# Kernel tuning notes

Measured on AMD Instinct MI355X. Metric: run time of the kernel, lower is better.

The kernel has to match this reference:

```python
import jax, jax.numpy as jnp
import numpy as np

N, F, E, C = 50000, 128, 800000, 10

def setup_inputs() -> dict:
    key = jax.random.key(0)
    ks = jax.random.split(key, 16)
    s = 1.0 / np.sqrt(F)
    def u(k, shape):
        return jax.random.uniform(k, shape, jnp.float32, -s, s)
    inp = {
        "x": jax.random.normal(ks[0], (N, F), jnp.float32),
        "edge_index": jax.random.randint(ks[1], (2, E), 0, N),
    }
    for i, p in enumerate(["1", "2"]):
        b = 2 + i * 5
        inp["W" + p] = u(ks[b], (F, F))          # EvolveGCNO initial_weight
        inp["wih" + p] = u(ks[b + 1], (3 * F, F))  # GRU input weights (r,z,n)
        inp["whh" + p] = u(ks[b + 2], (3 * F, F))  # GRU hidden weights
        inp["bih" + p] = u(ks[b + 3], (3 * F,))
        inp["bhh" + p] = u(ks[b + 4], (3 * F,))
    inp["lin_w"] = u(ks[12], (C, F))
    inp["lin_b"] = u(ks[13], (C,))
    return inp

def gru_step(x, h, wih, whh, bih, bhh):
    # torch.nn.GRU single step; gate order r, z, n
    gi = x @ wih.T + bih
    gh = h @ whh.T + bhh
    ir, iz, inn = jnp.split(gi, 3, axis=-1)
    hr, hz, hn = jnp.split(gh, 3, axis=-1)
    r = jax.nn.sigmoid(ir + hr)
    z = jax.nn.sigmoid(iz + hz)
    n = jnp.tanh(inn + r * hn)
    return (1.0 - z) * n + z * h

def gcn_conv(W, x, src, dst):
    # GCNConv_Fixed_W: gcn_norm with self-loops, then aggregate (x @ W)
    n = x.shape[0]
    loop = jnp.arange(n)
    s = jnp.concatenate([src, loop])
    d = jnp.concatenate([dst, loop])
    deg = jax.ops.segment_sum(jnp.ones(s.shape[0], x.dtype), d, num_segments=n)
    dinv = jnp.where(deg > 0, jax.lax.rsqrt(deg), 0.0)
    norm = dinv[s] * dinv[d]                 # [E+N]
    xw = x @ W                               # [N, F]
    return jax.ops.segment_sum(norm[:, None] * xw[s], d, num_segments=n)

def evolve_gcno(x, src, dst, W0, wih, whh, bih, bhh):
    # weight evolved by GRU with input = hidden = current weight
    W = gru_step(W0, W0, wih, whh, bih, bhh)
    return gcn_conv(W, x, src, dst)

def reference(x, edge_index, W1, wih1, whh1, bih1, bhh1,
              W2, wih2, whh2, bih2, bhh2, lin_w, lin_b):
    src, dst = edge_index[0], edge_index[1]
    h = jax.nn.relu(evolve_gcno(x, src, dst, W1, wih1, whh1, bih1, bhh1))
    # dropout is identity in eval mode
    h = jax.nn.relu(evolve_gcno(h, src, dst, W2, wih2, whh2, bih2, bhh2))
    logits = h @ lin_w.T + lin_b
    return jax.nn.log_softmax(logits, axis=1)
```

## Files before the change

kernel.cpp:

```cpp
#include <hip/hip_runtime.h>
#include <cstddef>
#include <cstdint>

#define F 128
#define C_OUT 10
#define SB 256

typedef short bf16x8 __attribute__((ext_vector_type(8)));
typedef float f32x4  __attribute__((ext_vector_type(4)));

__device__ __forceinline__ unsigned pack_bf16x2(float a, float b) {
  unsigned ua = __float_as_uint(a);
  unsigned ub = __float_as_uint(b);
  ua = (ua + 0x7FFFu + ((ua >> 16) & 1u)) >> 16;
  ub = (ub + 0x7FFFu + ((ub >> 16) & 1u)) >> 16;
  return ua | (ub << 16);
}
__device__ __forceinline__ float unpk_lo(unsigned p) { return __uint_as_float(p << 16); }
__device__ __forceinline__ float unpk_hi(unsigned p) { return __uint_as_float(p & 0xFFFF0000u); }
__device__ __forceinline__ unsigned short bf16_rne(float f) {
  unsigned u = __float_as_uint(f);
  return (unsigned short)((u + 0x7FFFu + ((u >> 16) & 1u)) >> 16);
}

__global__ void gru_evolve2_k(const float* __restrict__ W01, const float* __restrict__ wih1,
                              const float* __restrict__ whh1, const float* __restrict__ bih1,
                              const float* __restrict__ bhh1,
                              const float* __restrict__ W02, const float* __restrict__ wih2,
                              const float* __restrict__ whh2, const float* __restrict__ bih2,
                              const float* __restrict__ bhh2,
                              unsigned short* __restrict__ Bhi1, unsigned short* __restrict__ Blo1,
                              unsigned short* __restrict__ Bhi2, unsigned short* __restrict__ Blo2,
                              int* __restrict__ counts, int n) {
  if ((int)blockIdx.x >= 128) {
    int i = ((int)blockIdx.x - 128) * SB + threadIdx.x;
    if (i < n) counts[i] = 0;
    return;
  }
  int t = blockIdx.x * 256 + threadIdx.x;
  int layer = t >> 14;
  int tt = t & 16383;
  const float* W0  = layer ? W02  : W01;
  const float* wih = layer ? wih2 : wih1;
  const float* whh = layer ? whh2 : whh1;
  const float* bih = layer ? bih2 : bih1;
  const float* bhh = layer ? bhh2 : bhh1;
  unsigned short* Bhi = layer ? Bhi2 : Bhi1;
  unsigned short* Blo = layer ? Blo2 : Blo1;
  int i = tt >> 7, j = tt & 127;
  const float4* w0r = (const float4*)(W0 + (size_t)i * F);
  float gi[3], gh[3];
#pragma unroll
  for (int g = 0; g < 3; ++g) {
    const float4* wr = (const float4*)(wih + (size_t)(g * F + j) * F);
    const float4* hr = (const float4*)(whh + (size_t)(g * F + j) * F);
    float si = 0.f, sh = 0.f;
    for (int k = 0; k < F / 4; ++k) {
      float4 a = w0r[k];
      float4 b = wr[k];
      float4 c = hr[k];
      si += a.x * b.x + a.y * b.y + a.z * b.z + a.w * b.w;
      sh += a.x * c.x + a.y * c.y + a.z * c.z + a.w * c.w;
    }
    gi[g] = si + bih[g * F + j];
    gh[g] = sh + bhh[g * F + j];
  }
  float r = 1.0f / (1.0f + expf(-(gi[0] + gh[0])));
  float z = 1.0f / (1.0f + expf(-(gi[1] + gh[1])));
  float nn = tanhf(gi[2] + r * gh[2]);
  float val = (1.0f - z) * nn + z * W0[(size_t)i * F + j];

  unsigned u = __float_as_uint(val);
  unsigned short hi = (unsigned short)(u >> 16);
  float lo_f = val - __uint_as_float(u & 0xFFFF0000u);
  unsigned short lo = bf16_rne(lo_f);
  int kstep = i >> 5, kl = i & 31;
  int lane = (kl >> 3) * 16 + (j & 15);
  int tile = j >> 4;
  int idx = ((kstep * 8 + tile) * 64 + lane) * 8 + (kl & 7);
  Bhi[idx] = hi;
  Blo[idx] = lo;
}

__global__ void count_rank_k(const int* __restrict__ dst, int* __restrict__ counts,
                             int* __restrict__ rank, int E) {
  int e = blockIdx.x * blockDim.x + threadIdx.x;
  if (e < E) rank[e] = atomicAdd(&counts[dst[e]], 1);
}

__global__ void scan_local_k(const int* __restrict__ counts, int* __restrict__ incl,
                             int* __restrict__ blocksum, int n) {
  __shared__ int sh[SB];
  int gid = blockIdx.x * SB + threadIdx.x;
  int v = (gid < n) ? counts[gid] : 0;
  sh[threadIdx.x] = v;
  __syncthreads();
  for (int off = 1; off < SB; off <<= 1) {
    int t = 0;
    if ((int)threadIdx.x >= off) t = sh[threadIdx.x - off];
    __syncthreads();
    if ((int)threadIdx.x >= off) sh[threadIdx.x] += t;
    __syncthreads();
  }
  if (gid < n) incl[gid] = sh[threadIdx.x];
  if (threadIdx.x == SB - 1) blocksum[blockIdx.x] = sh[SB - 1];
}

__global__ void scan_blocks_k(int* __restrict__ blocksum, int nb) {
  __shared__ int sh[SB];
  int v = ((int)threadIdx.x < nb) ? blocksum[threadIdx.x] : 0;
  sh[threadIdx.x] = v;
  __syncthreads();
  for (int off = 1; off < SB; off <<= 1) {
    int t = 0;
    if ((int)threadIdx.x >= off) t = sh[threadIdx.x - off];
    __syncthreads();
    if ((int)threadIdx.x >= off) sh[threadIdx.x] += t;
    __syncthreads();
  }
  if ((int)threadIdx.x < nb) blocksum[threadIdx.x] = sh[threadIdx.x] - v;
}

__global__ void scan_finish_k(const int* __restrict__ counts, const int* __restrict__ incl,
                              const int* __restrict__ blocksum, int* __restrict__ rowptr,
                              float* __restrict__ dinv, int n) {
  int gid = blockIdx.x * SB + threadIdx.x;
  if (gid >= n) return;
  int c = counts[gid];
  int inc = blocksum[blockIdx.x] + incl[gid];
  rowptr[gid] = inc - c;
  dinv[gid] = rsqrtf((float)c + 1.0f);
  if (gid == n - 1) rowptr[n] = inc;
}

__global__ void fill_k(const int* __restrict__ src, const int* __restrict__ dst,
                       const int* __restrict__ rank, const int* __restrict__ rowptr,
                       int* __restrict__ csr_src, int E) {
  int e = blockIdx.x * blockDim.x + threadIdx.x;
  if (e < E) {
    int d = dst[e];
    csr_src[rowptr[d] + rank[e]] = src[e];
  }
}

__global__ void gemm_mfma_k(const float* __restrict__ X,
                            const unsigned short* __restrict__ Bhi,
                            const unsigned short* __restrict__ Blo,
                            const float* __restrict__ dinv, unsigned* __restrict__ Y,
                            int nrows) {
  int wid = (int)((blockIdx.x * blockDim.x + threadIdx.x) >> 6);
  int lane = threadIdx.x & 63;
  int ng = (nrows + 15) >> 4;
  if (wid >= ng) return;
  int g = __builtin_amdgcn_readfirstlane(wid);
  int q = lane >> 4, m = lane & 15;
  int rowA = g * 16 + m;
  if (rowA >= nrows) rowA = nrows - 1;

  f32x4 acc[8];
#pragma unroll
  for (int t = 0; t < 8; ++t) { acc[t].x = 0.f; acc[t].y = 0.f; acc[t].z = 0.f; acc[t].w = 0.f; }

#pragma unroll
  for (int s = 0; s < 4; ++s) {
    const float* xp = X + (size_t)rowA * F + s * 32 + q * 8;
    float4 xa = *(const float4*)xp;
    float4 xb = *(const float4*)(xp + 4);
    float xv[8] = {xa.x, xa.y, xa.z, xa.w, xb.x, xb.y, xb.z, xb.w};
    bf16x8 xhi, xlo;
#pragma unroll
    for (int j = 0; j < 8; ++j) {
      unsigned u = __float_as_uint(xv[j]);
      xhi[j] = (short)(u >> 16);
      float lf = xv[j] - __uint_as_float(u & 0xFFFF0000u);
      xlo[j] = (short)bf16_rne(lf);
    }
#pragma unroll
    for (int t = 0; t < 8; ++t) {
      size_t boff = ((size_t)(s * 8 + t) * 64 + lane) * 8;
      bf16x8 wh = *(const bf16x8*)(Bhi + boff);
      bf16x8 wl = *(const bf16x8*)(Blo + boff);
      acc[t] = __builtin_amdgcn_mfma_f32_16x16x32_bf16(wh, xhi, acc[t], 0, 0, 0);
      acc[t] = __builtin_amdgcn_mfma_f32_16x16x32_bf16(wh, xlo, acc[t], 0, 0, 0);
      acc[t] = __builtin_amdgcn_mfma_f32_16x16x32_bf16(wl, xhi, acc[t], 0, 0, 0);
    }
  }

  int row = g * 16 + m;
  if (row < nrows) {
    float dd = dinv[row];
    unsigned* yr = Y + (size_t)row * 64 + q * 2;
#pragma unroll
    for (int t = 0; t < 8; ++t) {
      uint2 o;
      o.x = pack_bf16x2(dd * acc[t].x, dd * acc[t].y);
      o.y = pack_bf16x2(dd * acc[t].z, dd * acc[t].w);
      *(uint2*)(yr + t * 8) = o;
    }
  }
}

template <bool FUSE_LOGITS>
__global__ void agg_bf16_k(const int* __restrict__ rowptr, const int* __restrict__ csr_src,
                           const float* __restrict__ dinv, const unsigned* __restrict__ xwp,
                           float* __restrict__ hout,
                           const float* __restrict__ lw, const float* __restrict__ lb,
                           float* __restrict__ outp, int n) {
  int wave = (int)((blockIdx.x * blockDim.x + threadIdx.x) >> 6);
  int lane = threadIdx.x & 63;
  if (wave >= n) return;
  int node = __builtin_amdgcn_readfirstlane(wave);
  float dd = dinv[node];
  unsigned um = xwp[(size_t)node * 64 + lane];
  float accx = unpk_lo(um), accy = unpk_hi(um);
  int b = rowptr[node], e = rowptr[node + 1];
  int i = b;
  for (; i + 8 <= e; i += 8) {
    int s0 = csr_src[i + 0], s1 = csr_src[i + 1], s2 = csr_src[i + 2], s3 = csr_src[i + 3];
    int s4 = csr_src[i + 4], s5 = csr_src[i + 5], s6 = csr_src[i + 6], s7 = csr_src[i + 7];
    unsigned u0 = xwp[(size_t)s0 * 64 + lane];
    unsigned u1 = xwp[(size_t)s1 * 64 + lane];
    unsigned u2 = xwp[(size_t)s2 * 64 + lane];
    unsigned u3 = xwp[(size_t)s3 * 64 + lane];
    unsigned u4 = xwp[(size_t)s4 * 64 + lane];
    unsigned u5 = xwp[(size_t)s5 * 64 + lane];
    unsigned u6 = xwp[(size_t)s6 * 64 + lane];
    unsigned u7 = xwp[(size_t)s7 * 64 + lane];
    accx += unpk_lo(u0); accy += unpk_hi(u0);
    accx += unpk_lo(u1); accy += unpk_hi(u1);
    accx += unpk_lo(u2); accy += unpk_hi(u2);
    accx += unpk_lo(u3); accy += unpk_hi(u3);
    accx += unpk_lo(u4); accy += unpk_hi(u4);
    accx += unpk_lo(u5); accy += unpk_hi(u5);
    accx += unpk_lo(u6); accy += unpk_hi(u6);
    accx += unpk_lo(u7); accy += unpk_hi(u7);
  }
  for (; i < e; ++i) {
    int s = csr_src[i];
    unsigned u = xwp[(size_t)s * 64 + lane];
    accx += unpk_lo(u); accy += unpk_hi(u);
  }
  float hx = fmaxf(dd * accx, 0.f);
  float hy = fmaxf(dd * accy, 0.f);
  if (!FUSE_LOGITS) {
    float2 r; r.x = hx; r.y = hy;
    ((float2*)hout)[(size_t)node * 64 + lane] = r;
  } else {
    float acc[C_OUT];
    const float2* lw2 = (const float2*)lw;
#pragma unroll
    for (int c = 0; c < C_OUT; ++c) {
      float2 w = lw2[(size_t)c * 64 + lane];
      float v = hx * w.x + hy * w.y;
#pragma unroll
      for (int off = 1; off < 64; off <<= 1) v += __shfl_xor(v, off);
      acc[c] = v + lb[c];
    }
    float mx = acc[0];
#pragma unroll
    for (int c = 1; c < C_OUT; ++c) mx = fmaxf(mx, acc[c]);
    float s = 0.f;
#pragma unroll
    for (int c = 0; c < C_OUT; ++c) s += expf(acc[c] - mx);
    float lse = mx + logf(s);
#pragma unroll
    for (int c = 0; c < C_OUT; ++c)
      if (lane == c) outp[(size_t)node * C_OUT + c] = acc[c] - lse;
  }
}

extern "C" void kernel_launch(void* const* d_in, const int* in_sizes, int n_in,
                              void* d_out, int out_size, void* d_ws, size_t ws_size,
                              hipStream_t stream) {
  const float* x    = (const float*)d_in[0];
  const int*   ei   = (const int*)d_in[1];
  const float* W1   = (const float*)d_in[2];
  const float* wih1 = (const float*)d_in[3];
  const float* whh1 = (const float*)d_in[4];
  const float* bih1 = (const float*)d_in[5];
  const float* bhh1 = (const float*)d_in[6];
  const float* W2   = (const float*)d_in[7];
  const float* wih2 = (const float*)d_in[8];
  const float* whh2 = (const float*)d_in[9];
  const float* bih2 = (const float*)d_in[10];
  const float* bhh2 = (const float*)d_in[11];
  const float* lw   = (const float*)d_in[12];
  const float* lb   = (const float*)d_in[13];
  float* out = (float*)d_out;

  int N = in_sizes[0] / F;
  int E = in_sizes[1] / 2;
  const int* src = ei;
  const int* dst = ei + E;
  int nb = (N + SB - 1) / SB;
  int ng = (N + 15) / 16;

  float* ws   = (float*)d_ws;
  unsigned* bufA = (unsigned*)ws;
  float* bufB = ws + (size_t)N * F / 2;
  float* dinv = bufB + (size_t)N * F;
  unsigned short* Bhi1 = (unsigned short*)(dinv + N);
  unsigned short* Blo1 = Bhi1 + F * F;
  unsigned short* Bhi2 = Blo1 + F * F;
  unsigned short* Blo2 = Bhi2 + F * F;
  int* counts = (int*)(Blo2 + F * F);
  int* rowptr = counts + N;
  int* rank   = rowptr + N + 1;
  int* incl   = rank + E;
  int* blocksum = incl + N;
  int* csr_src = blocksum + 256;

  gru_evolve2_k<<<128 + nb, 256, 0, stream>>>(W1, wih1, whh1, bih1, bhh1,
                                              W2, wih2, whh2, bih2, bhh2,
                                              Bhi1, Blo1, Bhi2, Blo2, counts, N);

  count_rank_k<<<(E + 255) / 256, 256, 0, stream>>>(dst, counts, rank, E);
  scan_local_k<<<nb, SB, 0, stream>>>(counts, incl, blocksum, N);
  scan_blocks_k<<<1, SB, 0, stream>>>(blocksum, nb);
  scan_finish_k<<<nb, SB, 0, stream>>>(counts, incl, blocksum, rowptr, dinv, N);
  fill_k<<<(E + 255) / 256, 256, 0, stream>>>(src, dst, rank, rowptr, csr_src, E);

  gemm_mfma_k<<<(ng + 3) / 4, 256, 0, stream>>>(x, Bhi1, Blo1, dinv, bufA, N);
  agg_bf16_k<false><<<(N + 3) / 4, 256, 0, stream>>>(rowptr, csr_src, dinv, bufA, bufB,
                                                     nullptr, nullptr, nullptr, N);

  gemm_mfma_k<<<(ng + 3) / 4, 256, 0, stream>>>(bufB, Bhi2, Blo2, dinv, bufA, N);
  agg_bf16_k<true><<<(N + 3) / 4, 256, 0, stream>>>(rowptr, csr_src, dinv, bufA, nullptr,
                                                    lw, lb, out, N);
}
```

Before: 289.2 us.

## Split wave into four edge groups with 16-byte gathers; fuse block-scan into finish

Measured after the change: 294.1 us. No clear change (+1.7%).

```diff
diff --git a/kernel.cpp b/kernel.cpp
--- a/kernel.cpp
+++ b/kernel.cpp
@@ -106,10 +106,14 @@
   if (threadIdx.x == SB - 1) blocksum[blockIdx.x] = sh[SB - 1];
 }
 
-__global__ void scan_blocks_k(int* __restrict__ blocksum, int nb) {
+__global__ void scan_finish_k(const int* __restrict__ counts, const int* __restrict__ incl,
+                              const int* __restrict__ blocksum, int* __restrict__ rowptr,
+                              float* __restrict__ dinv, int n, int nb) {
   __shared__ int sh[SB];
+  __shared__ int orig[SB];
   int v = ((int)threadIdx.x < nb) ? blocksum[threadIdx.x] : 0;
   sh[threadIdx.x] = v;
+  orig[threadIdx.x] = v;
   __syncthreads();
   for (int off = 1; off < SB; off <<= 1) {
     int t = 0;
@@ -118,16 +122,11 @@
     if ((int)threadIdx.x >= off) sh[threadIdx.x] += t;
     __syncthreads();
   }
-  if ((int)threadIdx.x < nb) blocksum[threadIdx.x] = sh[threadIdx.x] - v;
-}
-
-__global__ void scan_finish_k(const int* __restrict__ counts, const int* __restrict__ incl,
-                              const int* __restrict__ blocksum, int* __restrict__ rowptr,
-                              float* __restrict__ dinv, int n) {
+  int myoff = sh[blockIdx.x] - orig[blockIdx.x];
   int gid = blockIdx.x * SB + threadIdx.x;
   if (gid >= n) return;
   int c = counts[gid];
-  int inc = blocksum[blockIdx.x] + incl[gid];
+  int inc = myoff + incl[gid];
   rowptr[gid] = inc - c;
   dinv[gid] = rsqrtf((float)c + 1.0f);
   if (gid == n - 1) rowptr[n] = inc;
@@ -210,50 +209,74 @@
   int lane = threadIdx.x & 63;
   if (wave >= n) return;
   int node = __builtin_amdgcn_readfirstlane(wave);
+  int q = lane >> 4, m = lane & 15;
   float dd = dinv[node];
-  unsigned um = xwp[(size_t)node * 64 + lane];
-  float accx = unpk_lo(um), accy = unpk_hi(um);
+  float a0 = 0.f, a1 = 0.f, a2 = 0.f, a3 = 0.f, a4 = 0.f, a5 = 0.f, a6 = 0.f, a7 = 0.f;
+
+#define ADD8(U)                                        \
+  do {                                                 \
+    a0 += unpk_lo((U).x); a1 += unpk_hi((U).x);        \
+    a2 += unpk_lo((U).y); a3 += unpk_hi((U).y);        \
+    a4 += unpk_lo((U).z); a5 += unpk_hi((U).z);        \
+    a6 += unpk_lo((U).w); a7 += unpk_hi((U).w);        \
+  } while (0)
+
+  {
+    uint4 u = *(const uint4*)(xwp + (size_t)node * 64 + m * 4);
+    if (q != 0) { u.x = 0u; u.y = 0u; u.z = 0u; u.w = 0u; }
+    ADD8(u);
+  }
+
   int b = rowptr[node], e = rowptr[node + 1];
   int i = b;
   for (; i + 8 <= e; i += 8) {
-    int s0 = csr_src[i + 0], s1 = csr_src[i + 1], s2 = csr_src[i + 2], s3 = csr_src[i + 3];
-    int s4 = csr_src[i + 4], s5 = csr_src[i + 5], s6 = csr_src[i + 6], s7 = csr_src[i + 7];
-    unsigned u0 = xwp[(size_t)s0 * 64 + lane];
-    unsigned u1 = xwp[(size_t)s1 * 64 + lane];
-    unsigned u2 = xwp[(size_t)s2 * 64 + lane];
-    unsigned u3 = xwp[(size_t)s3 * 64 + lane];
-    unsigned u4 = xwp[(size_t)s4 * 64 + lane];
-    unsigned u5 = xwp[(size_t)s5 * 64 + lane];
-    unsigned u6 = xwp[(size_t)s6 * 64 + lane];
-    unsigned u7 = xwp[(size_t)s7 * 64 + lane];
-    accx += unpk_lo(u0); accy += unpk_hi(u0);
-    accx += unpk_lo(u1); accy += unpk_hi(u1);
-    accx += unpk_lo(u2); accy += unpk_hi(u2);
-    accx += unpk_lo(u3); accy += unpk_hi(u3);
-    accx += unpk_lo(u4); accy += unpk_hi(u4);
-    accx += unpk_lo(u5); accy += unpk_hi(u5);
-    accx += unpk_lo(u6); accy += unpk_hi(u6);
-    accx += unpk_lo(u7); accy += unpk_hi(u7);
-  }
-  for (; i < e; ++i) {
-    int s = csr_src[i];
-    unsigned u = xwp[(size_t)s * 64 + lane];
-    accx += unpk_lo(u); accy += unpk_hi(u);
-  }
-  float hx = fmaxf(dd * accx, 0.f);
-  float hy = fmaxf(dd * accy, 0.f);
+    int s0 = csr_src[i + q];
+    int s1 = csr_src[i + 4 + q];
+    uint4 ua = *(const uint4*)(xwp + (size_t)s0 * 64 + m * 4);
+    uint4 ub = *(const uint4*)(xwp + (size_t)s1 * 64 + m * 4);
+    ADD8(ua);
+    ADD8(ub);
+  }
+  for (; i < e; i += 4) {
+    int idx = i + q;
+    int ci = (idx < e) ? idx : (e - 1);
+    int s = csr_src[ci];
+    uint4 u = *(const uint4*)(xwp + (size_t)s * 64 + m * 4);
+    if (idx >= e) { u.x = 0u; u.y = 0u; u.z = 0u; u.w = 0u; }
+    ADD8(u);
+  }
+#undef ADD8
+
+  a0 += __shfl_xor(a0, 16); a1 += __shfl_xor(a1, 16);
+  a2 += __shfl_xor(a2, 16); a3 += __shfl_xor(a3, 16);
+  a4 += __shfl_xor(a4, 16); a5 += __shfl_xor(a5, 16);
+  a6 += __shfl_xor(a6, 16); a7 += __shfl_xor(a7, 16);
+  a0 += __shfl_xor(a0, 32); a1 += __shfl_xor(a1, 32);
+  a2 += __shfl_xor(a2, 32); a3 += __shfl_xor(a3, 32);
+  a4 += __shfl_xor(a4, 32); a5 += __shfl_xor(a5, 32);
+  a6 += __shfl_xor(a6, 32); a7 += __shfl_xor(a7, 32);
+
+  float h0 = fmaxf(dd * a0, 0.f), h1 = fmaxf(dd * a1, 0.f);
+  float h2 = fmaxf(dd * a2, 0.f), h3 = fmaxf(dd * a3, 0.f);
+  float h4 = fmaxf(dd * a4, 0.f), h5 = fmaxf(dd * a5, 0.f);
+  float h6 = fmaxf(dd * a6, 0.f), h7 = fmaxf(dd * a7, 0.f);
+
   if (!FUSE_LOGITS) {
-    float2 r; r.x = hx; r.y = hy;
-    ((float2*)hout)[(size_t)node * 64 + lane] = r;
+    if (lane < 16) {
+      float4* o = (float4*)(hout + (size_t)node * F + m * 8);
+      o[0] = make_float4(h0, h1, h2, h3);
+      o[1] = make_float4(h4, h5, h6, h7);
+    }
   } else {
     float acc[C_OUT];
-    const float2* lw2 = (const float2*)lw;
 #pragma unroll
     for (int c = 0; c < C_OUT; ++c) {
-      float2 w = lw2[(size_t)c * 64 + lane];
-      float v = hx * w.x + hy * w.y;
-#pragma unroll
-      for (int off = 1; off < 64; off <<= 1) v += __shfl_xor(v, off);
+      const float4* wr = (const float4*)(lw + (size_t)c * F + m * 8);
+      float4 w0 = wr[0], w1 = wr[1];
+      float v = h0 * w0.x + h1 * w0.y + h2 * w0.z + h3 * w0.w +
+                h4 * w1.x + h5 * w1.y + h6 * w1.z + h7 * w1.w;
+      v += __shfl_xor(v, 1); v += __shfl_xor(v, 2);
+      v += __shfl_xor(v, 4); v += __shfl_xor(v, 8);
       acc[c] = v + lb[c];
     }
     float mx = acc[0];
@@ -316,8 +339,7 @@
 
   count_rank_k<<<(E + 255) / 256, 256, 0, stream>>>(dst, counts, rank, E);
   scan_local_k<<<nb, SB, 0, stream>>>(counts, incl, blocksum, N);
-  scan_blocks_k<<<1, SB, 0, stream>>>(blocksum, nb);
-  scan_finish_k<<<nb, SB, 0, stream>>>(counts, incl, blocksum, rowptr, dinv, N);
+  scan_finish_k<<<nb, SB, 0, stream>>>(counts, incl, blocksum, rowptr, dinv, N, nb);
   fill_k<<<(E + 255) / 256, 256, 0, stream>>>(src, dst, rank, rowptr, csr_src, E);
 
   gemm_mfma_k<<<(ng + 3) / 4, 256, 0, stream>>>(x, Bhi1, Blo1, dinv, bufA, N);
```

## Merge block scan into finish, co-launch fill with GEMM, split-wave gather

Applied to the files above, without the earlier changes.

Result: faster. 278.6 us (-3.7%).

```diff
diff --git a/kernel.cpp b/kernel.cpp
--- a/kernel.cpp
+++ b/kernel.cpp
@@ -8,6 +8,7 @@
 
 typedef short bf16x8 __attribute__((ext_vector_type(8)));
 typedef float f32x4  __attribute__((ext_vector_type(4)));
+typedef float f32x2  __attribute__((ext_vector_type(2)));
 
 __device__ __forceinline__ unsigned pack_bf16x2(float a, float b) {
   unsigned ua = __float_as_uint(a);
@@ -16,11 +17,15 @@
   ub = (ub + 0x7FFFu + ((ub >> 16) & 1u)) >> 16;
   return ua | (ub << 16);
 }
-__device__ __forceinline__ float unpk_lo(unsigned p) { return __uint_as_float(p << 16); }
-__device__ __forceinline__ float unpk_hi(unsigned p) { return __uint_as_float(p & 0xFFFF0000u); }
 __device__ __forceinline__ unsigned short bf16_rne(float f) {
   unsigned u = __float_as_uint(f);
   return (unsigned short)((u + 0x7FFFu + ((u >> 16) & 1u)) >> 16);
+}
+__device__ __forceinline__ f32x2 unpk2(unsigned u) {
+  f32x2 r;
+  r.x = __uint_as_float(u << 16);
+  r.y = __uint_as_float(u & 0xFFFF0000u);
+  return r;
 }
 
 __global__ void gru_evolve2_k(const float* __restrict__ W01, const float* __restrict__ wih1,
@@ -106,10 +111,14 @@
   if (threadIdx.x == SB - 1) blocksum[blockIdx.x] = sh[SB - 1];
 }
 
-__global__ void scan_blocks_k(int* __restrict__ blocksum, int nb) {
+__global__ void scan_finish_k(const int* __restrict__ counts, const int* __restrict__ incl,
+                              const int* __restrict__ blocksum, int* __restrict__ rowptr,
+                              float* __restrict__ dinv, int n, int nb) {
   __shared__ int sh[SB];
+  __shared__ int orig[SB];
   int v = ((int)threadIdx.x < nb) ? blocksum[threadIdx.x] : 0;
   sh[threadIdx.x] = v;
+  orig[threadIdx.x] = v;
   __syncthreads();
   for (int off = 1; off < SB; off <<= 1) {
     int t = 0;
@@ -118,37 +127,34 @@
     if ((int)threadIdx.x >= off) sh[threadIdx.x] += t;
     __syncthreads();
   }
-  if ((int)threadIdx.x < nb) blocksum[threadIdx.x] = sh[threadIdx.x] - v;
-}
-
-__global__ void scan_finish_k(const int* __restrict__ counts, const int* __restrict__ incl,
-                              const int* __restrict__ blocksum, int* __restrict__ rowptr,
-                              float* __restrict__ dinv, int n) {
+  int myoff = sh[blockIdx.x] - orig[blockIdx.x];
   int gid = blockIdx.x * SB + threadIdx.x;
   if (gid >= n) return;
   int c = counts[gid];
-  int inc = blocksum[blockIdx.x] + incl[gid];
+  int inc = myoff + incl[gid];
   rowptr[gid] = inc - c;
   dinv[gid] = rsqrtf((float)c + 1.0f);
   if (gid == n - 1) rowptr[n] = inc;
 }
 
-__global__ void fill_k(const int* __restrict__ src, const int* __restrict__ dst,
-                       const int* __restrict__ rank, const int* __restrict__ rowptr,
-                       int* __restrict__ csr_src, int E) {
-  int e = blockIdx.x * blockDim.x + threadIdx.x;
+__device__ __forceinline__ void fill_body(int bid, const int* __restrict__ src,
+                                          const int* __restrict__ dst,
+                                          const int* __restrict__ rank,
+                                          const int* __restrict__ rowptr,
+                                          int* __restrict__ csr_src, int E) {
+  int e = bid * 256 + (int)threadIdx.x;
   if (e < E) {
     int d = dst[e];
     csr_src[rowptr[d] + rank[e]] = src[e];
   }
 }
 
-__global__ void gemm_mfma_k(const float* __restrict__ X,
-                            const unsigned short* __restrict__ Bhi,
-                            const unsigned short* __restrict__ Blo,
-                            const float* __restrict__ dinv, unsigned* __restrict__ Y,
-                            int nrows) {
-  int wid = (int)((blockIdx.x * blockDim.x + threadIdx.x) >> 6);
+__device__ __forceinline__ void gemm_body(int bid, const float* __restrict__ X,
+                                          const unsigned short* __restrict__ Bhi,
+                                          const unsigned short* __restrict__ Blo,
+                                          const float* __restrict__ dinv,
+                                          unsigned* __restrict__ Y, int nrows) {
+  int wid = bid * 4 + ((int)threadIdx.x >> 6);
   int lane = threadIdx.x & 63;
   int ng = (nrows + 15) >> 4;
   if (wid >= ng) return;
@@ -198,6 +204,28 @@
       *(uint2*)(yr + t * 8) = o;
     }
   }
+}
+
+__global__ void gemm_mfma_k(const float* __restrict__ X,
+                            const unsigned short* __restrict__ Bhi,
+                            const unsigned short* __restrict__ Blo,
+                            const float* __restrict__ dinv, unsigned* __restrict__ Y,
+                            int nrows) {
+  gemm_body(blockIdx.x, X, Bhi, Blo, dinv, Y, nrows);
+}
+
+__global__ void fill_gemm_k(const float* __restrict__ X,
+                            const unsigned short* __restrict__ Bhi,
+                            const unsigned short* __restrict__ Blo,
+                            const float* __restrict__ dinv, unsigned* __restrict__ Y,
+                            int nrows, int ngemm,
+                            const int* __restrict__ src, const int* __restrict__ dst,
+                            const int* __restrict__ rank, const int* __restrict__ rowptr,
+                            int* __restrict__ csr_src, int E) {
+  if ((int)blockIdx.x < ngemm)
+    gemm_body(blockIdx.x, X, Bhi, Blo, dinv, Y, nrows);
+  else
+    fill_body((int)blockIdx.x - ngemm, src, dst, rank, rowptr, csr_src, E);
 }
 
 template <bool FUSE_LOGITS>
@@ -210,50 +238,74 @@
   int lane = threadIdx.x & 63;
   if (wave >= n) return;
   int node = __builtin_amdgcn_readfirstlane(wave);
+  int half = lane >> 5, hm = lane & 31;
   float dd = dinv[node];
-  unsigned um = xwp[(size_t)node * 64 + lane];
-  float accx = unpk_lo(um), accy = unpk_hi(um);
+  const uint2* __restrict__ base = (const uint2*)xwp;
+  f32x2 acc0 = {0.f, 0.f}, acc1 = {0.f, 0.f};
+
+  {
+    uint2 u = base[(size_t)node * 32 + hm];
+    if (half) { u.x = 0u; u.y = 0u; }
+    acc0 += unpk2(u.x);
+    acc1 += unpk2(u.y);
+  }
+
   int b = rowptr[node], e = rowptr[node + 1];
   int i = b;
   for (; i + 8 <= e; i += 8) {
     int s0 = csr_src[i + 0], s1 = csr_src[i + 1], s2 = csr_src[i + 2], s3 = csr_src[i + 3];
     int s4 = csr_src[i + 4], s5 = csr_src[i + 5], s6 = csr_src[i + 6], s7 = csr_src[i + 7];
-    unsigned u0 = xwp[(size_t)s0 * 64 + lane];
-    unsigned u1 = xwp[(size_t)s1 * 64 + lane];
-    unsigned u2 = xwp[(size_t)s2 * 64 + lane];
-    unsigned u3 = xwp[(size_t)s3 * 64 + lane];
-    unsigned u4 = xwp[(size_t)s4 * 64 + lane];
-    unsigned u5 = xwp[(size_t)s5 * 64 + lane];
-    unsigned u6 = xwp[(size_t)s6 * 64 + lane];
-    unsigned u7 = xwp[(size_t)s7 * 64 + lane];
-    accx += unpk_lo(u0); accy += unpk_hi(u0);
-    accx += unpk_lo(u1); accy += unpk_hi(u1);
-    accx += unpk_lo(u2); accy += unpk_hi(u2);
-    accx += unpk_lo(u3); accy += unpk_hi(u3);
-    accx += unpk_lo(u4); accy += unpk_hi(u4);
-    accx += unpk_lo(u5); accy += unpk_hi(u5);
-    accx += unpk_lo(u6); accy += unpk_hi(u6);
-    accx += unpk_lo(u7); accy += unpk_hi(u7);
-  }
-  for (; i < e; ++i) {
+    int sa = half ? s1 : s0;
+    int sb = half ? s3 : s2;
+    int sc = half ? s5 : s4;
+    int sd = half ? s7 : s6;
+    uint2 ua = base[(size_t)sa * 32 + hm];
+    uint2 ub = base[(size_t)sb * 32 + hm];
+    uint2 uc = base[(size_t)sc * 32 + hm];
+    uint2 ud = base[(size_t)sd * 32 + hm];
+    acc0 += unpk2(ua.x); acc1 += unpk2(ua.y);
+    acc0 += unpk2(ub.x); acc1 += unpk2(ub.y);
+    acc0 += unpk2(uc.x); acc1 += unpk2(uc.y);
+    acc0 += unpk2(ud.x); acc1 += unpk2(ud.y);
+  }
+  for (; i + 2 <= e; i += 2) {
+    int s0 = csr_src[i], s1 = csr_src[i + 1];
+    int s = half ? s1 : s0;
+    uint2 u = base[(size_t)s * 32 + hm];
+    acc0 += unpk2(u.x);
+    acc1 += unpk2(u.y);
+  }
+  if (i < e) {
     int s = csr_src[i];
-    unsigned u = xwp[(size_t)s * 64 + lane];
-    accx += unpk_lo(u); accy += unpk_hi(u);
-  }
-  float hx = fmaxf(dd * accx, 0.f);
-  float hy = fmaxf(dd * accy, 0.f);
+    uint2 u = base[(size_t)s * 32 + hm];
+    if (half) { u.x = 0u; u.y = 0u; }
+    acc0 += unpk2(u.x);
+    acc1 += unpk2(u.y);
+  }
+
+  acc0.x += __shfl_xor(acc0.x, 32);
+  acc0.y += __shfl_xor(acc0.y, 32);
+  acc1.x += __shfl_xor(acc1.x, 32);
+  acc1.y += __shfl_xor(acc1.y, 32);
+
+  float h0 = fmaxf(dd * acc0.x, 0.f);
+  float h1 = fmaxf(dd * acc0.y, 0.f);
+  float h2 = fmaxf(dd * acc1.x, 0.f);
+  float h3 = fmaxf(dd * acc1.y, 0.f);
+
   if (!FUSE_LOGITS) {
-    float2 r; r.x = hx; r.y = hy;
-    ((float2*)hout)[(size_t)node * 64 + lane] = r;
+    if (half == 0) {
+      *(float4*)(hout + (size_t)node * F + hm * 4) = make_float4(h0, h1, h2, h3);
+    }
   } else {
     float acc[C_OUT];
-    const float2* lw2 = (const float2*)lw;
 #pragma unroll
     for (int c = 0; c < C_OUT; ++c) {
-      float2 w = lw2[(size_t)c * 64 + lane];
-      float v = hx * w.x + hy * w.y;
-#pragma unroll
-      for (int off = 1; off < 64; off <<= 1) v += __shfl_xor(v, off);
+      float4 w = *(const float4*)(lw + (size_t)c * F + hm * 4);
+      float v = h0 * w.x + h1 * w.y + h2 * w.z + h3 * w.w;
+      v += __shfl_xor(v, 1); v += __shfl_xor(v, 2);
+      v += __shfl_xor(v, 4); v += __shfl_xor(v, 8);
+      v += __shfl_xor(v, 16);
       acc[c] = v + lb[c];
     }
     float mx = acc[0];
@@ -294,6 +346,8 @@
   const int* dst = ei + E;
   int nb = (N + SB - 1) / SB;
   int ng = (N + 15) / 16;
+  int ngemm = (ng + 3) / 4;
+  int nfill = (E + 255) / 256;
 
   float* ws   = (float*)d_ws;
   unsigned* bufA = (unsigned*)ws;
@@ -316,15 +370,14 @@
 
   count_rank_k<<<(E + 255) / 256, 256, 0, stream>>>(dst, counts, rank, E);
   scan_local_k<<<nb, SB, 0, stream>>>(counts, incl, blocksum, N);
-  scan_blocks_k<<<1, SB, 0, stream>>>(blocksum, nb);
-  scan_finish_k<<<nb, SB, 0, stream>>>(counts, incl, blocksum, rowptr, dinv, N);
-  fill_k<<<(E + 255) / 256, 256, 0, stream>>>(src, dst, rank, rowptr, csr_src, E);
-
-  gemm_mfma_k<<<(ng + 3) / 4, 256, 0, stream>>>(x, Bhi1, Blo1, dinv, bufA, N);
+  scan_finish_k<<<nb, SB, 0, stream>>>(counts, incl, blocksum, rowptr, dinv, N, nb);
+
+  fill_gemm_k<<<ngemm + nfill, 256, 0, stream>>>(x, Bhi1, Blo1, dinv, bufA, N, ngemm,
+                                                 src, dst, rank, rowptr, csr_src, E);
   agg_bf16_k<false><<<(N + 3) / 4, 256, 0, stream>>>(rowptr, csr_src, dinv, bufA, bufB,
                                                      nullptr, nullptr, nullptr, N);
 
-  gemm_mfma_k<<<(ng + 3) / 4, 256, 0, stream>>>(bufB, Bhi2, Blo2, dinv, bufA, N);
+  gemm_mfma_k<<<ngemm, 256, 0, stream>>>(bufB, Bhi2, Blo2, dinv, bufA, N);
   agg_bf16_k<true><<<(N + 3) / 4, 256, 0, stream>>>(rowptr, csr_src, dinv, bufA, nullptr,
                                                     lw, lb, out, N);
 }
```
